# Optimization experiments

Hardware: AMD Instinct MI355X
Metric: run time of the kernel (lower is better)

Reference implementation:

```python
import jax, jax.numpy as jnp
import numpy as np

BLUR = 0.05
P = 2
EPS_FINAL = BLUR ** P          # geomloss: eps = blur**p = 0.0025
DIAMETER = 2.0                 # max cosine cost magnitude
SCALING = 0.5                  # geomloss default; eps decays by scaling**p per step
N_FINAL_ITERS = 4              # extra balancing iterations at the final eps


def eps_schedule():
    eps_list = []
    e = DIAMETER ** P
    while e > EPS_FINAL:
        eps_list.append(e)
        e = e * (SCALING ** P)
    eps_list.extend([EPS_FINAL] * N_FINAL_ITERS)
    return eps_list


def cosine_cost(a, b):
    # a: (N, D), b: (M, D) -> (N, M) cost = 1 - cos_sim
    an = a / (jnp.linalg.norm(a, axis=1, keepdims=True) + 1e-12)
    bn = b / (jnp.linalg.norm(b, axis=1, keepdims=True) + 1e-12)
    return 1.0 - an @ bn.T


def softmin(C, pot, log_w, eps):
    # -eps * LSE_j( log_w + (pot_j - C_ij)/eps ) ; C: (N, M), pot: (M,)
    return -eps * jax.nn.logsumexp(log_w + (pot[None, :] - C) / eps, axis=1)


def sinkhorn_divergence(Cxy, Cxx, Cyy):
    N, M = Cxy.shape
    log_a = -jnp.log(jnp.asarray(N, dtype=Cxy.dtype))  # uniform weights
    log_b = -jnp.log(jnp.asarray(M, dtype=Cxy.dtype))
    sg = jax.lax.stop_gradient
    # Sinkhorn iterations run on detached costs (geomloss envelope-theorem trick)
    Cxy_s, Cxx_s, Cyy_s = sg(Cxy), sg(Cxx), sg(Cyy)
    f = jnp.zeros((N,), Cxy.dtype)
    g = jnp.zeros((M,), Cxy.dtype)
    fxx = jnp.zeros((N,), Cxy.dtype)
    gyy = jnp.zeros((M,), Cxy.dtype)
    for eps in eps_schedule():
        # symmetric (debiasing) potentials: averaged fixed-point update
        fxx = 0.5 * (fxx + softmin(Cxx_s, fxx, log_a, eps))
        gyy = 0.5 * (gyy + softmin(Cyy_s, gyy, log_b, eps))
        # cross potentials: simultaneous (Jacobi) update
        f, g = softmin(Cxy_s, g, log_b, eps), softmin(Cxy_s.T, f, log_a, eps)
    # final extrapolation step with gradients flowing through the costs
    eps = EPS_FINAL
    f_fin = softmin(Cxy, sg(g), log_b, eps)
    g_fin = softmin(Cxy.T, sg(f), log_a, eps)
    fxx_fin = softmin(Cxx, sg(fxx), log_a, eps)
    gyy_fin = softmin(Cyy, sg(gyy), log_b, eps)
    return jnp.mean(f_fin - fxx_fin) + jnp.mean(g_fin - gyy_fin)


def setup_inputs() -> dict:
    key = jax.random.key(0)
    k1, k2, k3 = jax.random.split(key, 3)
    x1 = jax.random.normal(k1, (8192, 256), dtype=jnp.float32)
    x2 = jax.random.normal(k2, (8192, 256), dtype=jnp.float32)
    w = jax.random.uniform(k3, (256,), dtype=jnp.float32)
    return {"x1": x1, "x2": x2, "w": w}


def reference(x1, x2, w):
    # Dist_loss.forward: clamp+renormalize learned per-feature weights, scale x1
    w_c = jnp.clip(w, 0.0, 2.0)
    w_c = w_c / jnp.mean(w_c)
    a = w_c[None, :] * x1
    Cxy = cosine_cost(a, x2)
    Cxx = cosine_cost(a, a)
    Cyy = cosine_cost(x2, x2)
    return sinkhorn_divergence(Cxy, Cxx, Cyy)
```

## Files before the change

kernel.cpp:

```cpp
#include <hip/hip_runtime.h>
#include <math.h>

#define N 8192
#define D 256
#define LN2 0.6931471805599453f
#define LDSROW 280
#define TSLOTS 1152

typedef short short8 __attribute__((ext_vector_type(8)));
typedef float f32x16 __attribute__((ext_vector_type(16)));
typedef unsigned short ushort;

__device__ __forceinline__ float fexp2(float x) { return __builtin_amdgcn_exp2f(x); }
__device__ __forceinline__ float flog2(float x) { return __builtin_amdgcn_logf(x); }

__device__ __forceinline__ ushort bf16r(float x) {
    unsigned int u = __float_as_uint(x);
    return (ushort)((u + 0x7FFF + ((u >> 16) & 1)) >> 16);
}

__device__ __forceinline__ void gl_lds16(const ushort* g, ushort* l) {
    __builtin_amdgcn_global_load_lds(
        (const __attribute__((address_space(1))) unsigned int*)g,
        (__attribute__((address_space(3))) unsigned int*)l, 16, 0, 0);
}

__global__ void prep_wc(const float* __restrict__ w, float* __restrict__ wc) {
    int t = threadIdx.x;
    float v = fminf(fmaxf(w[t], 0.0f), 2.0f);
    float s = v;
#pragma unroll
    for (int m = 1; m < 64; m <<= 1) s += __shfl_xor(s, m);
    __shared__ float sm[4];
    if ((t & 63) == 0) sm[t >> 6] = s;
    __syncthreads();
    float mean = (sm[0] + sm[1] + sm[2] + sm[3]) * (1.0f / 256.0f);
    wc[t] = v / mean;
}

__global__ void prep_normalize(const float* __restrict__ x1, const float* __restrict__ x2,
                               const float* __restrict__ wc,
                               ushort* __restrict__ an_i, ushort* __restrict__ bn_i) {
    int row = blockIdx.x;
    int t = threadIdx.x;
    int r; float v; ushort* ip;
    if (row < N) { r = row;     v = x1[(size_t)r * D + t] * wc[t]; ip = an_i; }
    else         { r = row - N; v = x2[(size_t)r * D + t];         ip = bn_i; }
    float ss = v * v;
#pragma unroll
    for (int m = 1; m < 64; m <<= 1) ss += __shfl_xor(ss, m);
    __shared__ float sm[4];
    if ((t & 63) == 0) sm[t >> 6] = ss;
    __syncthreads();
    float denom = sqrtf(sm[0] + sm[1] + sm[2] + sm[3]) + 1e-12f;
    ip[(size_t)r * D + t] = bf16r(v / denom);
}

__global__ void init_pots(float* __restrict__ pots, float* __restrict__ potm1) {
    int id = blockIdx.x * 256 + threadIdx.x;
    pots[id] = 0.0f;
    potm1[id] = -1.0f;
}

__global__ __launch_bounds__(128, 2) void softmin_mfma(
    const ushort* __restrict__ an_i, const ushort* __restrict__ bn_i,
    const float* __restrict__ potm1,
    float2* __restrict__ parts, float k1) {
    int bx = blockIdx.x;
    int k = bx & 7;
    int q = bx >> 3;
    int task = k >> 1;
    int split = ((k & 1) << 1) | (q >> 6);
    int rb = q & 63;
    const ushort* jp = (task == 0 || task == 3) ? an_i : bn_i;
    const ushort* ip = (task == 0 || task == 2) ? an_i : bn_i;
    const float* pm1 = potm1 + (size_t)task * N;

    int t = threadIdx.x;
    int wave = t >> 6, lane = t & 63;
    int l31 = lane & 31, lh = lane >> 5;
    int i0 = rb * 128 + wave * 64;

    __shared__ ushort lbuf[2][TSLOTS * 8];

    short8 bi0[16], bi1[16];
    {
        const ushort* ib = ip + (size_t)(i0 + l31) * D + lh * 8;
#pragma unroll
        for (int c = 0; c < 16; ++c) {
            bi0[c] = *(const short8*)(ib + c * 16);
            bi1[c] = *(const short8*)(ib + (size_t)32 * D + c * 16);
        }
    }
#pragma unroll
    for (int c = 0; c < 16; ++c) {
        asm volatile("" : "+a"(bi0[c]), "+a"(bi1[c]));
    }

    const int jbase0 = split * 2048;

    int offA[9];
    int offP = 0;
    bool tail = false;
#pragma unroll
    for (int r = 0; r < 9; ++r) {
        int s = r * 128 + t;
        if (s >= 1120) {
            int u = s - 1120;
            offP = (u > 7 ? 7 : u) * 8;
            tail = true;
            offA[r] = 0;
        } else {
            int row = s / 35;
            int c = s - row * 35;
            c = c > 31 ? 31 : c;
            offA[r] = row * D + c * 8;
        }
    }

    auto stage = [&](int b, int js) {
        int j0 = jbase0 + js * 32;
        const ushort* gb = jp + (size_t)j0 * D;
        const ushort* gp = (const ushort*)(pm1 + j0);
        ushort* lb = &lbuf[b][0];
#pragma unroll
        for (int r = 0; r < 8; ++r)
            gl_lds16(gb + offA[r], lb + (r * 128 + t) * 8);
        gl_lds16(tail ? gp + offP : gb + offA[8], lb + (1024 + t) * 8);
    };

    auto tile = [&](const ushort* lb, f32x16& c0, f32x16& c1) {
        const float* pl = (const float*)(lb + 1120 * 8);
        float4 p0 = *(const float4*)&pl[4 * lh + 0];
        float4 p1 = *(const float4*)&pl[4 * lh + 8];
        float4 p2 = *(const float4*)&pl[4 * lh + 16];
        float4 p3 = *(const float4*)&pl[4 * lh + 24];
        c0[0] = p0.x; c0[1] = p0.y; c0[2]  = p0.z; c0[3]  = p0.w;
        c0[4] = p1.x; c0[5] = p1.y; c0[6]  = p1.z; c0[7]  = p1.w;
        c0[8] = p2.x; c0[9] = p2.y; c0[10] = p2.z; c0[11] = p2.w;
        c0[12] = p3.x; c0[13] = p3.y; c0[14] = p3.z; c0[15] = p3.w;
        c1 = c0;
        const ushort* lrow = lb + l31 * LDSROW + lh * 8;
        __builtin_amdgcn_s_setprio(1);
#pragma unroll
        for (int c = 0; c < 16; ++c) {
            short8 af = *(const short8*)(lrow + c * 16);
            c0 = __builtin_amdgcn_mfma_f32_32x32x16_bf16(af, bi0[c], c0, 0, 0, 0);
            c1 = __builtin_amdgcn_mfma_f32_32x32x16_bf16(af, bi1[c], c1, 0, 0, 0);
        }
        __builtin_amdgcn_s_setprio(0);
    };

    float m0 = -INFINITY, s0 = 0.0f, m1 = -INFINITY, s1 = 0.0f;

    auto lse = [&](const f32x16& c, float& m, float& s) {
        float a01 = fmaxf(c[0], c[1]),   a23 = fmaxf(c[2], c[3]);
        float a45 = fmaxf(c[4], c[5]),   a67 = fmaxf(c[6], c[7]);
        float a89 = fmaxf(c[8], c[9]),   aab = fmaxf(c[10], c[11]);
        float acd = fmaxf(c[12], c[13]), aef = fmaxf(c[14], c[15]);
        float q0 = fmaxf(a01, a23), q1 = fmaxf(a45, a67);
        float q2 = fmaxf(a89, aab), q3 = fmaxf(acd, aef);
        float mx = fmaxf(fmaxf(q0, q1), fmaxf(q2, q3));
        float mn = fmaxf(m, mx * k1);
        float nm = -mn;
        float t0 = fexp2(fmaf(c[0],  k1, nm)) + fexp2(fmaf(c[1],  k1, nm));
        float t1 = fexp2(fmaf(c[2],  k1, nm)) + fexp2(fmaf(c[3],  k1, nm));
        float t2 = fexp2(fmaf(c[4],  k1, nm)) + fexp2(fmaf(c[5],  k1, nm));
        float t3 = fexp2(fmaf(c[6],  k1, nm)) + fexp2(fmaf(c[7],  k1, nm));
        float t4 = fexp2(fmaf(c[8],  k1, nm)) + fexp2(fmaf(c[9],  k1, nm));
        float t5 = fexp2(fmaf(c[10], k1, nm)) + fexp2(fmaf(c[11], k1, nm));
        float t6 = fexp2(fmaf(c[12], k1, nm)) + fexp2(fmaf(c[13], k1, nm));
        float t7 = fexp2(fmaf(c[14], k1, nm)) + fexp2(fmaf(c[15], k1, nm));
        float ad = ((t0 + t1) + (t2 + t3)) + ((t4 + t5) + (t6 + t7));
        s = fmaf(s, fexp2(m - mn), ad);
        m = mn;
    };

    f32x16 a0, a1;

    stage(0, 0);
    for (int js = 0; js < 64; ++js) {
        int cur = js & 1;
        __syncthreads();
        if (js < 63) stage(cur ^ 1, js + 1);
        tile(&lbuf[cur][0], a0, a1);
        lse(a0, m0, s0);
        lse(a1, m1, s1);
    }

    float mo = __shfl_xor(m0, 32), so = __shfl_xor(s0, 32);
    float M0 = fmaxf(m0, mo);
    float S0 = s0 * fexp2(m0 - M0) + so * fexp2(mo - M0);
    mo = __shfl_xor(m1, 32); so = __shfl_xor(s1, 32);
    float M1 = fmaxf(m1, mo);
    float S1 = s1 * fexp2(m1 - M1) + so * fexp2(mo - M1);
    if (lane < 32) {
        size_t r0 = (size_t)task * N + (i0 + l31);
        size_t r1 = r0 + 32;
        parts[r0 * 4 + split] = make_float2(M0, S0);
        parts[r1 * 4 + split] = make_float2(M1, S1);
    }
}

__global__ void merge_pots(const float2* __restrict__ parts, float* __restrict__ pots,
                           float* __restrict__ potm1, float eps, float logw, int do_avg) {
    int id = blockIdx.x * 256 + threadIdx.x;
    int task = id >> 13;
    int row = id & (N - 1);
    const float2* p = parts + (size_t)id * 4;
    float2 a = p[0], b = p[1], c = p[2], d = p[3];
    float M = fmaxf(fmaxf(a.x, b.x), fmaxf(c.x, d.x));
    float S = a.y * fexp2(a.x - M) + b.y * fexp2(b.x - M) +
              c.y * fexp2(c.x - M) + d.y * fexp2(d.x - M);
    float lse = LN2 * (M + flog2(S));
    float v = -eps * (logw + lse);
    if (do_avg && task < 2) v = 0.5f * (pots[id] + v);
    pots[id] = v;
    int ct = (task < 2) ? task : (5 - task);
    potm1[(size_t)ct * N + row] = v - 1.0f;
}

__global__ void final_reduce(const float* __restrict__ pots, float* __restrict__ out) {
    int t = threadIdx.x;
    float s = 0.0f;
    for (int i = t; i < N; i += 256)
        s += (pots[2 * N + i] - pots[i]) + (pots[3 * N + i] - pots[N + i]);
#pragma unroll
    for (int m = 1; m < 64; m <<= 1) s += __shfl_xor(s, m);
    __shared__ float sm[4];
    if ((t & 63) == 0) sm[t >> 6] = s;
    __syncthreads();
    if (t == 0) out[0] = (sm[0] + sm[1] + sm[2] + sm[3]) * (1.0f / (float)N);
}

extern "C" void kernel_launch(void* const* d_in, const int* in_sizes, int n_in,
                              void* d_out, int out_size, void* d_ws, size_t ws_size,
                              hipStream_t stream) {
    const float* x1 = (const float*)d_in[0];
    const float* x2 = (const float*)d_in[1];
    const float* w  = (const float*)d_in[2];
    float* out = (float*)d_out;

    ushort* an_i = (ushort*)d_ws;
    ushort* bn_i = an_i + (size_t)N * D;
    float*  wc   = (float*)(bn_i + (size_t)N * D);
    float*  pots = wc + 256;
    float*  potm1 = pots + 4 * N;
    float2* parts = (float2*)(potm1 + 4 * N);

    prep_wc<<<1, 256, 0, stream>>>(w, wc);
    prep_normalize<<<2 * N, 256, 0, stream>>>(x1, x2, wc, an_i, bn_i);
    init_pots<<<4 * N / 256, 256, 0, stream>>>(pots, potm1);

    const float eps_list[10] = {4.0f, 1.0f, 0.25f, 0.0625f, 0.015625f,
                                0.00390625f, 0.0025f, 0.0025f, 0.0025f, 0.0025f};
    const float logw = -logf((float)N);
    const float LOG2E = 1.4426950408889634f;
    for (int it = 0; it < 10; ++it) {
        softmin_mfma<<<1024, 128, 0, stream>>>(an_i, bn_i, potm1, parts, LOG2E / eps_list[it]);
        merge_pots<<<4 * N / 256, 256, 0, stream>>>(parts, pots, potm1,
                                                    eps_list[it], logw, 1);
    }
    softmin_mfma<<<1024, 128, 0, stream>>>(an_i, bn_i, potm1, parts, LOG2E / 0.0025f);
    merge_pots<<<4 * N / 256, 256, 0, stream>>>(parts, pots, potm1, 0.0025f, logw, 0);
    final_reduce<<<1, 256, 0, stream>>>(pots, out);
}
```

Before: 1.683 ms.

## Warp-specialize softmin: MFMA waves write tiles to LDS, consumer waves do LSE

The block grows from 128 to 256 threads and the waves are split into two roles. Producer waves stage J tiles and run the MFMA matmul, then write the accumulator tiles into a double-buffered LDS region. Consumer waves read the previous tile from LDS and compute the streaming log-sum-exp. The goal is to overlap the exp-heavy LSE with matrix-core work across waves. The cost is extra LDS traffic, more shared memory per block and one extra pipeline step.

```diff
diff --git a/kernel.cpp b/kernel.cpp
--- a/kernel.cpp
+++ b/kernel.cpp
@@ -5,7 +5,7 @@
 #define D 256
 #define LN2 0.6931471805599453f
 #define LDSROW 280
-#define TSLOTS 1152
+#define JBUF_USH 9216
 
 typedef short short8 __attribute__((ext_vector_type(8)));
 typedef float f32x16 __attribute__((ext_vector_type(16)));
@@ -62,7 +62,7 @@
     potm1[id] = -1.0f;
 }
 
-__global__ __launch_bounds__(128, 2) void softmin_mfma(
+__global__ __launch_bounds__(256, 2) void softmin_mfma(
     const ushort* __restrict__ an_i, const ushort* __restrict__ bn_i,
     const float* __restrict__ potm1,
     float2* __restrict__ parts, float k1) {
@@ -79,54 +79,55 @@
     int t = threadIdx.x;
     int wave = t >> 6, lane = t & 63;
     int l31 = lane & 31, lh = lane >> 5;
-    int i0 = rb * 128 + wave * 64;
-
-    __shared__ ushort lbuf[2][TSLOTS * 8];
+    int pid = wave & 1;
+    int role = ((wave >> 1) ^ bx) & 1;
+    int i0 = rb * 128 + pid * 64;
+
+    __shared__ __attribute__((aligned(16))) ushort ldsA[38912];
+    float* accL = (float*)(ldsA + 2 * JBUF_USH);
+
+    const int jbase0 = split * 2048;
 
     short8 bi0[16], bi1[16];
-    {
+    int offA[9]; int offP = 0; bool tail = false;
+    int tp = pid * 64 + lane;
+
+    if (role == 0) {
         const ushort* ib = ip + (size_t)(i0 + l31) * D + lh * 8;
 #pragma unroll
         for (int c = 0; c < 16; ++c) {
             bi0[c] = *(const short8*)(ib + c * 16);
             bi1[c] = *(const short8*)(ib + (size_t)32 * D + c * 16);
         }
-    }
-#pragma unroll
-    for (int c = 0; c < 16; ++c) {
-        asm volatile("" : "+a"(bi0[c]), "+a"(bi1[c]));
-    }
-
-    const int jbase0 = split * 2048;
-
-    int offA[9];
-    int offP = 0;
-    bool tail = false;
-#pragma unroll
-    for (int r = 0; r < 9; ++r) {
-        int s = r * 128 + t;
-        if (s >= 1120) {
-            int u = s - 1120;
-            offP = (u > 7 ? 7 : u) * 8;
-            tail = true;
-            offA[r] = 0;
-        } else {
-            int row = s / 35;
-            int c = s - row * 35;
-            c = c > 31 ? 31 : c;
-            offA[r] = row * D + c * 8;
-        }
-    }
-
-    auto stage = [&](int b, int js) {
+#pragma unroll
+        for (int c = 0; c < 16; ++c) {
+            asm volatile("" : "+a"(bi0[c]), "+a"(bi1[c]));
+        }
+#pragma unroll
+        for (int r = 0; r < 9; ++r) {
+            int s = r * 128 + tp;
+            if (s >= 1120) {
+                int u = s - 1120;
+                offP = (u > 7 ? 7 : u) * 8;
+                tail = true;
+                offA[r] = 0;
+            } else {
+                int row = s / 35;
+                int c = s - row * 35;
+                c = c > 31 ? 31 : c;
+                offA[r] = row * D + c * 8;
+            }
+        }
+    }
+
+    auto stage = [&](ushort* lb, int js) {
         int j0 = jbase0 + js * 32;
         const ushort* gb = jp + (size_t)j0 * D;
         const ushort* gp = (const ushort*)(pm1 + j0);
-        ushort* lb = &lbuf[b][0];
 #pragma unroll
         for (int r = 0; r < 8; ++r)
-            gl_lds16(gb + offA[r], lb + (r * 128 + t) * 8);
-        gl_lds16(tail ? gp + offP : gb + offA[8], lb + (1024 + t) * 8);
+            gl_lds16(gb + offA[r], lb + (r * 128 + tp) * 8);
+        gl_lds16(tail ? gp + offP : gb + offA[8], lb + (1024 + tp) * 8);
     };
 
     auto tile = [&](const ushort* lb, f32x16& c0, f32x16& c1) {
@@ -151,54 +152,76 @@
         __builtin_amdgcn_s_setprio(0);
     };
 
-    float m0 = -INFINITY, s0 = 0.0f, m1 = -INFINITY, s1 = 0.0f;
-
-    auto lse = [&](const f32x16& c, float& m, float& s) {
-        float a01 = fmaxf(c[0], c[1]),   a23 = fmaxf(c[2], c[3]);
-        float a45 = fmaxf(c[4], c[5]),   a67 = fmaxf(c[6], c[7]);
-        float a89 = fmaxf(c[8], c[9]),   aab = fmaxf(c[10], c[11]);
-        float acd = fmaxf(c[12], c[13]), aef = fmaxf(c[14], c[15]);
-        float q0 = fmaxf(a01, a23), q1 = fmaxf(a45, a67);
-        float q2 = fmaxf(a89, aab), q3 = fmaxf(acd, aef);
-        float mx = fmaxf(fmaxf(q0, q1), fmaxf(q2, q3));
+    auto lse_l = [&](const float* lp, float& m, float& s) {
+        float4 v0 = *(const float4*)(lp + 0);
+        float4 v1 = *(const float4*)(lp + 4);
+        float4 v2 = *(const float4*)(lp + 8);
+        float4 v3 = *(const float4*)(lp + 12);
+        float g0 = fmaxf(fmaxf(v0.x, v0.y), v0.z);
+        float g1 = fmaxf(fmaxf(v0.w, v1.x), v1.y);
+        float g2 = fmaxf(fmaxf(v1.z, v1.w), v2.x);
+        float g3 = fmaxf(fmaxf(v2.y, v2.z), v2.w);
+        float g4 = fmaxf(fmaxf(v3.x, v3.y), v3.z);
+        float mx = fmaxf(fmaxf(fmaxf(g0, g1), g2), fmaxf(fmaxf(g3, g4), v3.w));
         float mn = fmaxf(m, mx * k1);
         float nm = -mn;
-        float t0 = fexp2(fmaf(c[0],  k1, nm)) + fexp2(fmaf(c[1],  k1, nm));
-        float t1 = fexp2(fmaf(c[2],  k1, nm)) + fexp2(fmaf(c[3],  k1, nm));
-        float t2 = fexp2(fmaf(c[4],  k1, nm)) + fexp2(fmaf(c[5],  k1, nm));
-        float t3 = fexp2(fmaf(c[6],  k1, nm)) + fexp2(fmaf(c[7],  k1, nm));
-        float t4 = fexp2(fmaf(c[8],  k1, nm)) + fexp2(fmaf(c[9],  k1, nm));
-        float t5 = fexp2(fmaf(c[10], k1, nm)) + fexp2(fmaf(c[11], k1, nm));
-        float t6 = fexp2(fmaf(c[12], k1, nm)) + fexp2(fmaf(c[13], k1, nm));
-        float t7 = fexp2(fmaf(c[14], k1, nm)) + fexp2(fmaf(c[15], k1, nm));
+        float t0 = fexp2(fmaf(v0.x, k1, nm)) + fexp2(fmaf(v0.y, k1, nm));
+        float t1 = fexp2(fmaf(v0.z, k1, nm)) + fexp2(fmaf(v0.w, k1, nm));
+        float t2 = fexp2(fmaf(v1.x, k1, nm)) + fexp2(fmaf(v1.y, k1, nm));
+        float t3 = fexp2(fmaf(v1.z, k1, nm)) + fexp2(fmaf(v1.w, k1, nm));
+        float t4 = fexp2(fmaf(v2.x, k1, nm)) + fexp2(fmaf(v2.y, k1, nm));
+        float t5 = fexp2(fmaf(v2.z, k1, nm)) + fexp2(fmaf(v2.w, k1, nm));
+        float t6 = fexp2(fmaf(v3.x, k1, nm)) + fexp2(fmaf(v3.y, k1, nm));
+        float t7 = fexp2(fmaf(v3.z, k1, nm)) + fexp2(fmaf(v3.w, k1, nm));
         float ad = ((t0 + t1) + (t2 + t3)) + ((t4 + t5) + (t6 + t7));
         s = fmaf(s, fexp2(m - mn), ad);
         m = mn;
     };
 
-    f32x16 a0, a1;
-
-    stage(0, 0);
-    for (int js = 0; js < 64; ++js) {
-        int cur = js & 1;
+    float* aw = accL + pid * 2560 + lane * 20;
+
+    float m0 = -INFINITY, s0 = 0.0f, m1 = -INFINITY, s1 = 0.0f;
+
+    if (role == 0) stage(ldsA, 0);
+    for (int s = 0; s <= 64; ++s) {
         __syncthreads();
-        if (js < 63) stage(cur ^ 1, js + 1);
-        tile(&lbuf[cur][0], a0, a1);
-        lse(a0, m0, s0);
-        lse(a1, m1, s1);
-    }
-
-    float mo = __shfl_xor(m0, 32), so = __shfl_xor(s0, 32);
-    float M0 = fmaxf(m0, mo);
-    float S0 = s0 * fexp2(m0 - M0) + so * fexp2(mo - M0);
-    mo = __shfl_xor(m1, 32); so = __shfl_xor(s1, 32);
-    float M1 = fmaxf(m1, mo);
-    float S1 = s1 * fexp2(m1 - M1) + so * fexp2(mo - M1);
-    if (lane < 32) {
-        size_t r0 = (size_t)task * N + (i0 + l31);
-        size_t r1 = r0 + 32;
-        parts[r0 * 4 + split] = make_float2(M0, S0);
-        parts[r1 * 4 + split] = make_float2(M1, S1);
+        if (role == 0) {
+            if (s < 64) {
+                ushort* lb = ldsA + (s & 1) * JBUF_USH;
+                if (s < 63) stage(ldsA + ((s + 1) & 1) * JBUF_USH, s + 1);
+                f32x16 c0, c1;
+                tile(lb, c0, c1);
+                float* w = aw + (s & 1) * 5120;
+                *(float4*)(w + 0)  = make_float4(c0[0],  c0[1],  c0[2],  c0[3]);
+                *(float4*)(w + 4)  = make_float4(c0[4],  c0[5],  c0[6],  c0[7]);
+                *(float4*)(w + 8)  = make_float4(c0[8],  c0[9],  c0[10], c0[11]);
+                *(float4*)(w + 12) = make_float4(c0[12], c0[13], c0[14], c0[15]);
+                float* w1 = w + 1280;
+                *(float4*)(w1 + 0)  = make_float4(c1[0],  c1[1],  c1[2],  c1[3]);
+                *(float4*)(w1 + 4)  = make_float4(c1[4],  c1[5],  c1[6],  c1[7]);
+                *(float4*)(w1 + 8)  = make_float4(c1[8],  c1[9],  c1[10], c1[11]);
+                *(float4*)(w1 + 12) = make_float4(c1[12], c1[13], c1[14], c1[15]);
+            }
+        } else if (s >= 1) {
+            const float* r = aw + ((s - 1) & 1) * 5120;
+            lse_l(r, m0, s0);
+            lse_l(r + 1280, m1, s1);
+        }
+    }
+
+    if (role == 1) {
+        float mo = __shfl_xor(m0, 32), so = __shfl_xor(s0, 32);
+        float M0 = fmaxf(m0, mo);
+        float S0 = s0 * fexp2(m0 - M0) + so * fexp2(mo - M0);
+        mo = __shfl_xor(m1, 32); so = __shfl_xor(s1, 32);
+        float M1 = fmaxf(m1, mo);
+        float S1 = s1 * fexp2(m1 - M1) + so * fexp2(mo - M1);
+        if (lane < 32) {
+            size_t r0 = (size_t)task * N + (i0 + l31);
+            size_t r1 = r0 + 32;
+            parts[r0 * 4 + split] = make_float2(M0, S0);
+            parts[r1 * 4 + split] = make_float2(M1, S1);
+        }
     }
 }
 
@@ -257,11 +280,11 @@
     const float logw = -logf((float)N);
     const float LOG2E = 1.4426950408889634f;
     for (int it = 0; it < 10; ++it) {
-        softmin_mfma<<<1024, 128, 0, stream>>>(an_i, bn_i, potm1, parts, LOG2E / eps_list[it]);
+        softmin_mfma<<<1024, 256, 0, stream>>>(an_i, bn_i, potm1, parts, LOG2E / eps_list[it]);
         merge_pots<<<4 * N / 256, 256, 0, stream>>>(parts, pots, potm1,
                                                     eps_list[it], logw, 1);
     }
-    softmin_mfma<<<1024, 128, 0, stream>>>(an_i, bn_i, potm1, parts, LOG2E / 0.0025f);
+    softmin_mfma<<<1024, 256, 0, stream>>>(an_i, bn_i, potm1, parts, LOG2E / 0.0025f);
     merge_pots<<<4 * N / 256, 256, 0, stream>>>(parts, pots, potm1, 0.0025f, logw, 0);
     final_reduce<<<1, 256, 0, stream>>>(pots, out);
 }
```

New measurement: 2.138 ms. +27.0%, slower.

## Pre-swizzle operands into MFMA fragment layout and load directly from global

Applied to the files above, without the earlier changes.

The normalize kernel now writes the bf16 matrices in a tiled layout that matches the MFMA operand fragments, so each lane can read its short8 fragments with coalesced global loads. The softmin kernel drops the LDS double-buffer, the global_load_lds staging and the per-tile barriers, and register-prefetches the next tile's A fragments and potentials while the current tile's LSE runs. Blocks grow to 256 threads covering 256 rows, so the grid halves. This removes LDS traffic and synchronisation, but each wave now fetches the shared j-tile separately through L1/L2, and the extra 16 prefetched fragment registers raise register pressure.

```diff
diff --git a/kernel.cpp b/kernel.cpp
--- a/kernel.cpp
+++ b/kernel.cpp
@@ -4,8 +4,6 @@
 #define N 8192
 #define D 256
 #define LN2 0.6931471805599453f
-#define LDSROW 280
-#define TSLOTS 1152
 
 typedef short short8 __attribute__((ext_vector_type(8)));
 typedef float f32x16 __attribute__((ext_vector_type(16)));
@@ -19,12 +17,6 @@
     return (ushort)((u + 0x7FFF + ((u >> 16) & 1)) >> 16);
 }
 
-__device__ __forceinline__ void gl_lds16(const ushort* g, ushort* l) {
-    __builtin_amdgcn_global_load_lds(
-        (const __attribute__((address_space(1))) unsigned int*)g,
-        (__attribute__((address_space(3))) unsigned int*)l, 16, 0, 0);
-}
-
 __global__ void prep_wc(const float* __restrict__ w, float* __restrict__ wc) {
     int t = threadIdx.x;
     float v = fminf(fmaxf(w[t], 0.0f), 2.0f);
@@ -40,12 +32,12 @@
 
 __global__ void prep_normalize(const float* __restrict__ x1, const float* __restrict__ x2,
                                const float* __restrict__ wc,
-                               ushort* __restrict__ an_i, ushort* __restrict__ bn_i) {
+                               ushort* __restrict__ an_t, ushort* __restrict__ bn_t) {
     int row = blockIdx.x;
     int t = threadIdx.x;
     int r; float v; ushort* ip;
-    if (row < N) { r = row;     v = x1[(size_t)r * D + t] * wc[t]; ip = an_i; }
-    else         { r = row - N; v = x2[(size_t)r * D + t];         ip = bn_i; }
+    if (row < N) { r = row;     v = x1[(size_t)r * D + t] * wc[t]; ip = an_t; }
+    else         { r = row - N; v = x2[(size_t)r * D + t];         ip = bn_t; }
     float ss = v * v;
 #pragma unroll
     for (int m = 1; m < 64; m <<= 1) ss += __shfl_xor(ss, m);
@@ -53,7 +45,15 @@
     if ((t & 63) == 0) sm[t >> 6] = ss;
     __syncthreads();
     float denom = sqrtf(sm[0] + sm[1] + sm[2] + sm[3]) + 1e-12f;
-    ip[(size_t)r * D + t] = bf16r(v / denom);
+    __shared__ __attribute__((aligned(16))) ushort ls[256];
+    ls[t] = bf16r(v / denom);
+    __syncthreads();
+    if (t < 32) {
+        int c = t >> 1, lh = t & 1;
+        short8 vv = *(const short8*)&ls[c * 16 + lh * 8];
+        size_t base = (size_t)(r >> 5) * 8192 + (size_t)c * 512 + lh * 256 + (r & 31) * 8;
+        *(short8*)(ip + base) = vv;
+    }
 }
 
 __global__ void init_pots(float* __restrict__ pots, float* __restrict__ potm1) {
@@ -62,34 +62,32 @@
     potm1[id] = -1.0f;
 }
 
-__global__ __launch_bounds__(128, 2) void softmin_mfma(
-    const ushort* __restrict__ an_i, const ushort* __restrict__ bn_i,
+__global__ __launch_bounds__(256, 2) void softmin_mfma(
+    const ushort* __restrict__ an_t, const ushort* __restrict__ bn_t,
     const float* __restrict__ potm1,
     float2* __restrict__ parts, float k1) {
     int bx = blockIdx.x;
     int k = bx & 7;
     int q = bx >> 3;
     int task = k >> 1;
-    int split = ((k & 1) << 1) | (q >> 6);
-    int rb = q & 63;
-    const ushort* jp = (task == 0 || task == 3) ? an_i : bn_i;
-    const ushort* ip = (task == 0 || task == 2) ? an_i : bn_i;
+    int split = ((k & 1) << 1) | (q & 1);
+    int rb = q >> 1;
+    const ushort* jp = (task == 0 || task == 3) ? an_t : bn_t;
+    const ushort* ip = (task == 0 || task == 2) ? an_t : bn_t;
     const float* pm1 = potm1 + (size_t)task * N;
 
     int t = threadIdx.x;
     int wave = t >> 6, lane = t & 63;
     int l31 = lane & 31, lh = lane >> 5;
-    int i0 = rb * 128 + wave * 64;
-
-    __shared__ ushort lbuf[2][TSLOTS * 8];
+    int i0 = rb * 256 + wave * 64;
 
     short8 bi0[16], bi1[16];
     {
-        const ushort* ib = ip + (size_t)(i0 + l31) * D + lh * 8;
+        const ushort* ib = ip + (size_t)(i0 >> 5) * 8192 + lane * 8;
 #pragma unroll
         for (int c = 0; c < 16; ++c) {
-            bi0[c] = *(const short8*)(ib + c * 16);
-            bi1[c] = *(const short8*)(ib + (size_t)32 * D + c * 16);
+            bi0[c] = *(const short8*)(ib + c * 512);
+            bi1[c] = *(const short8*)(ib + 8192 + c * 512);
         }
     }
 #pragma unroll
@@ -98,69 +96,39 @@
     }
 
     const int jbase0 = split * 2048;
-
-    int offA[9];
-    int offP = 0;
-    bool tail = false;
-#pragma unroll
-    for (int r = 0; r < 9; ++r) {
-        int s = r * 128 + t;
-        if (s >= 1120) {
-            int u = s - 1120;
-            offP = (u > 7 ? 7 : u) * 8;
-            tail = true;
-            offA[r] = 0;
-        } else {
-            int row = s / 35;
-            int c = s - row * 35;
-            c = c > 31 ? 31 : c;
-            offA[r] = row * D + c * 8;
-        }
-    }
-
-    auto stage = [&](int b, int js) {
-        int j0 = jbase0 + js * 32;
-        const ushort* gb = jp + (size_t)j0 * D;
-        const ushort* gp = (const ushort*)(pm1 + j0);
-        ushort* lb = &lbuf[b][0];
-#pragma unroll
-        for (int r = 0; r < 8; ++r)
-            gl_lds16(gb + offA[r], lb + (r * 128 + t) * 8);
-        gl_lds16(tail ? gp + offP : gb + offA[8], lb + (1024 + t) * 8);
+    const ushort* ab = jp + (size_t)(jbase0 >> 5) * 8192 + lane * 8;
+    const float*  pb = pm1 + jbase0 + 4 * lh;
+
+    f32x16 c0, c1;
+    short8 af[16];
+
+    auto ldaf = [&]() {
+#pragma unroll
+        for (int c = 0; c < 16; ++c)
+            af[c] = *(const short8*)(ab + c * 512);
     };
-
-    auto tile = [&](const ushort* lb, f32x16& c0, f32x16& c1) {
-        const float* pl = (const float*)(lb + 1120 * 8);
-        float4 p0 = *(const float4*)&pl[4 * lh + 0];
-        float4 p1 = *(const float4*)&pl[4 * lh + 8];
-        float4 p2 = *(const float4*)&pl[4 * lh + 16];
-        float4 p3 = *(const float4*)&pl[4 * lh + 24];
+    auto ldpot = [&]() {
+        float4 p0 = *(const float4*)(pb + 0);
+        float4 p1 = *(const float4*)(pb + 8);
+        float4 p2 = *(const float4*)(pb + 16);
+        float4 p3 = *(const float4*)(pb + 24);
         c0[0] = p0.x; c0[1] = p0.y; c0[2]  = p0.z; c0[3]  = p0.w;
         c0[4] = p1.x; c0[5] = p1.y; c0[6]  = p1.z; c0[7]  = p1.w;
         c0[8] = p2.x; c0[9] = p2.y; c0[10] = p2.z; c0[11] = p2.w;
         c0[12] = p3.x; c0[13] = p3.y; c0[14] = p3.z; c0[15] = p3.w;
         c1 = c0;
-        const ushort* lrow = lb + l31 * LDSROW + lh * 8;
-        __builtin_amdgcn_s_setprio(1);
-#pragma unroll
-        for (int c = 0; c < 16; ++c) {
-            short8 af = *(const short8*)(lrow + c * 16);
-            c0 = __builtin_amdgcn_mfma_f32_32x32x16_bf16(af, bi0[c], c0, 0, 0, 0);
-            c1 = __builtin_amdgcn_mfma_f32_32x32x16_bf16(af, bi1[c], c1, 0, 0, 0);
-        }
-        __builtin_amdgcn_s_setprio(0);
     };
 
     float m0 = -INFINITY, s0 = 0.0f, m1 = -INFINITY, s1 = 0.0f;
 
     auto lse = [&](const f32x16& c, float& m, float& s) {
-        float a01 = fmaxf(c[0], c[1]),   a23 = fmaxf(c[2], c[3]);
-        float a45 = fmaxf(c[4], c[5]),   a67 = fmaxf(c[6], c[7]);
-        float a89 = fmaxf(c[8], c[9]),   aab = fmaxf(c[10], c[11]);
-        float acd = fmaxf(c[12], c[13]), aef = fmaxf(c[14], c[15]);
-        float q0 = fmaxf(a01, a23), q1 = fmaxf(a45, a67);
-        float q2 = fmaxf(a89, aab), q3 = fmaxf(acd, aef);
-        float mx = fmaxf(fmaxf(q0, q1), fmaxf(q2, q3));
+        float g0 = fmaxf(fmaxf(c[0],  c[1]),  c[2]);
+        float g1 = fmaxf(fmaxf(c[3],  c[4]),  c[5]);
+        float g2 = fmaxf(fmaxf(c[6],  c[7]),  c[8]);
+        float g3 = fmaxf(fmaxf(c[9],  c[10]), c[11]);
+        float g4 = fmaxf(fmaxf(c[12], c[13]), c[14]);
+        float h  = fmaxf(fmaxf(g0, g1), g2);
+        float mx = fmaxf(fmaxf(h, g3), fmaxf(g4, c[15]));
         float mn = fmaxf(m, mx * k1);
         float nm = -mn;
         float t0 = fexp2(fmaf(c[0],  k1, nm)) + fexp2(fmaf(c[1],  k1, nm));
@@ -176,16 +144,23 @@
         m = mn;
     };
 
-    f32x16 a0, a1;
-
-    stage(0, 0);
+    ldpot();
+    ldaf();
     for (int js = 0; js < 64; ++js) {
-        int cur = js & 1;
-        __syncthreads();
-        if (js < 63) stage(cur ^ 1, js + 1);
-        tile(&lbuf[cur][0], a0, a1);
-        lse(a0, m0, s0);
-        lse(a1, m1, s1);
+        __builtin_amdgcn_s_setprio(1);
+#pragma unroll
+        for (int c = 0; c < 16; ++c) {
+            short8 a = af[c];
+            c0 = __builtin_amdgcn_mfma_f32_32x32x16_bf16(a, bi0[c], c0, 0, 0, 0);
+            c1 = __builtin_amdgcn_mfma_f32_32x32x16_bf16(a, bi1[c], c1, 0, 0, 0);
+        }
+        __builtin_amdgcn_s_setprio(0);
+        ab += 8192;
+        if (js < 63) ldaf();
+        lse(c0, m0, s0);
+        lse(c1, m1, s1);
+        pb += 32;
+        if (js < 63) ldpot();
     }
 
     float mo = __shfl_xor(m0, 32), so = __shfl_xor(s0, 32);
@@ -241,15 +216,15 @@
     const float* w  = (const float*)d_in[2];
     float* out = (float*)d_out;
 
-    ushort* an_i = (ushort*)d_ws;
-    ushort* bn_i = an_i + (size_t)N * D;
-    float*  wc   = (float*)(bn_i + (size_t)N * D);
+    ushort* an_t = (ushort*)d_ws;
+    ushort* bn_t = an_t + (size_t)N * D;
+    float*  wc   = (float*)(bn_t + (size_t)N * D);
     float*  pots = wc + 256;
     float*  potm1 = pots + 4 * N;
     float2* parts = (float2*)(potm1 + 4 * N);
 
     prep_wc<<<1, 256, 0, stream>>>(w, wc);
-    prep_normalize<<<2 * N, 256, 0, stream>>>(x1, x2, wc, an_i, bn_i);
+    prep_normalize<<<2 * N, 256, 0, stream>>>(x1, x2, wc, an_t, bn_t);
     init_pots<<<4 * N / 256, 256, 0, stream>>>(pots, potm1);
 
     const float eps_list[10] = {4.0f, 1.0f, 0.25f, 0.0625f, 0.015625f,
@@ -257,11 +232,11 @@
     const float logw = -logf((float)N);
     const float LOG2E = 1.4426950408889634f;
     for (int it = 0; it < 10; ++it) {
-        softmin_mfma<<<1024, 128, 0, stream>>>(an_i, bn_i, potm1, parts, LOG2E / eps_list[it]);
+        softmin_mfma<<<512, 256, 0, stream>>>(an_t, bn_t, potm1, parts, LOG2E / eps_list[it]);
         merge_pots<<<4 * N / 256, 256, 0, stream>>>(parts, pots, potm1,
                                                     eps_list[it], logw, 1);
     }
-    softmin_mfma<<<1024, 128, 0, stream>>>(an_i, bn_i, potm1, parts, LOG2E / 0.0025f);
+    softmin_mfma<<<512, 256, 0, stream>>>(an_t, bn_t, potm1, parts, LOG2E / 0.0025f);
     merge_pots<<<4 * N / 256, 256, 0, stream>>>(parts, pots, potm1, 0.0025f, logw, 0);
     final_reduce<<<1, 256, 0, stream>>>(pots, out);
 }
```

New measurement: 1.793 ms. 6.6% more time.

## Enlarge softmin blocks to 8 waves, split MFMA chains, stagger LSE across wave groups

Applied to the files above, without the earlier changes.

Blocks grow from 128 to 512 threads (8 waves, 512 i-rows each), so each LDS-staged j tile is shared by four times as many waves and the grid shrinks to 256 blocks. The 16-step MFMA accumulation is split into two independent chains that are summed at the end, which shortens the dependency latency. Half the waves run their exp/LSE for the previous tile before issuing the next MFMAs, so matrix and vector work from different waves can interleave. The cost is more registers and fewer blocks in flight, and with only 256 blocks some CUs may sit idle.

```diff
diff --git a/kernel.cpp b/kernel.cpp
--- a/kernel.cpp
+++ b/kernel.cpp
@@ -62,7 +62,7 @@
     potm1[id] = -1.0f;
 }
 
-__global__ __launch_bounds__(128, 2) void softmin_mfma(
+__global__ __launch_bounds__(512, 2) void softmin_mfma(
     const ushort* __restrict__ an_i, const ushort* __restrict__ bn_i,
     const float* __restrict__ potm1,
     float2* __restrict__ parts, float k1) {
@@ -70,8 +70,8 @@
     int k = bx & 7;
     int q = bx >> 3;
     int task = k >> 1;
-    int split = ((k & 1) << 1) | (q >> 6);
-    int rb = q & 63;
+    int split = ((k & 1) << 1) | (q >> 4);
+    int rb = q & 15;
     const ushort* jp = (task == 0 || task == 3) ? an_i : bn_i;
     const ushort* ip = (task == 0 || task == 2) ? an_i : bn_i;
     const float* pm1 = potm1 + (size_t)task * N;
@@ -79,7 +79,8 @@
     int t = threadIdx.x;
     int wave = t >> 6, lane = t & 63;
     int l31 = lane & 31, lh = lane >> 5;
-    int i0 = rb * 128 + wave * 64;
+    int ga = (wave >> 2) == 0;
+    int i0 = rb * 512 + wave * 64;
 
     __shared__ ushort lbuf[2][TSLOTS * 8];
 
@@ -99,12 +100,12 @@
 
     const int jbase0 = split * 2048;
 
-    int offA[9];
+    int offA[3];
     int offP = 0;
     bool tail = false;
 #pragma unroll
-    for (int r = 0; r < 9; ++r) {
-        int s = r * 128 + t;
+    for (int r = 0; r < 3; ++r) {
+        int s = (r < 2) ? (r * 512 + t) : (1024 + (t & 127));
         if (s >= 1120) {
             int u = s - 1120;
             offP = (u > 7 ? 7 : u) * 8;
@@ -123,32 +124,48 @@
         const ushort* gb = jp + (size_t)j0 * D;
         const ushort* gp = (const ushort*)(pm1 + j0);
         ushort* lb = &lbuf[b][0];
-#pragma unroll
-        for (int r = 0; r < 8; ++r)
-            gl_lds16(gb + offA[r], lb + (r * 128 + t) * 8);
-        gl_lds16(tail ? gp + offP : gb + offA[8], lb + (1024 + t) * 8);
+        gl_lds16(gb + offA[0], lb + t * 8);
+        gl_lds16(gb + offA[1], lb + (512 + t) * 8);
+        gl_lds16(tail ? gp + offP : gb + offA[2], lb + (1024 + (t & 127)) * 8);
     };
 
-    auto tile = [&](const ushort* lb, f32x16& c0, f32x16& c1) {
+    f32x16 zz = {};
+    asm volatile("" : "+v"(zz));
+
+    auto chainsum = [&](const ushort* lb, f32x16& p0, f32x16& p1) {
         const float* pl = (const float*)(lb + 1120 * 8);
-        float4 p0 = *(const float4*)&pl[4 * lh + 0];
-        float4 p1 = *(const float4*)&pl[4 * lh + 8];
-        float4 p2 = *(const float4*)&pl[4 * lh + 16];
-        float4 p3 = *(const float4*)&pl[4 * lh + 24];
-        c0[0] = p0.x; c0[1] = p0.y; c0[2]  = p0.z; c0[3]  = p0.w;
-        c0[4] = p1.x; c0[5] = p1.y; c0[6]  = p1.z; c0[7]  = p1.w;
-        c0[8] = p2.x; c0[9] = p2.y; c0[10] = p2.z; c0[11] = p2.w;
-        c0[12] = p3.x; c0[13] = p3.y; c0[14] = p3.z; c0[15] = p3.w;
-        c1 = c0;
+        f32x16 pt;
+        float4 q0 = *(const float4*)&pl[4 * lh + 0];
+        float4 q1 = *(const float4*)&pl[4 * lh + 8];
+        float4 q2 = *(const float4*)&pl[4 * lh + 16];
+        float4 q3 = *(const float4*)&pl[4 * lh + 24];
+        pt[0] = q0.x; pt[1] = q0.y; pt[2]  = q0.z; pt[3]  = q0.w;
+        pt[4] = q1.x; pt[5] = q1.y; pt[6]  = q1.z; pt[7]  = q1.w;
+        pt[8] = q2.x; pt[9] = q2.y; pt[10] = q2.z; pt[11] = q2.w;
+        pt[12] = q3.x; pt[13] = q3.y; pt[14] = q3.z; pt[15] = q3.w;
         const ushort* lrow = lb + l31 * LDSROW + lh * 8;
+        f32x16 c0a, c0b, c1a, c1b;
         __builtin_amdgcn_s_setprio(1);
-#pragma unroll
-        for (int c = 0; c < 16; ++c) {
-            short8 af = *(const short8*)(lrow + c * 16);
-            c0 = __builtin_amdgcn_mfma_f32_32x32x16_bf16(af, bi0[c], c0, 0, 0, 0);
-            c1 = __builtin_amdgcn_mfma_f32_32x32x16_bf16(af, bi1[c], c1, 0, 0, 0);
+        {
+            short8 alo = *(const short8*)(lrow + 0);
+            short8 ahi = *(const short8*)(lrow + 8 * 16);
+            c0a = __builtin_amdgcn_mfma_f32_32x32x16_bf16(alo, bi0[0], pt, 0, 0, 0);
+            c1a = __builtin_amdgcn_mfma_f32_32x32x16_bf16(alo, bi1[0], pt, 0, 0, 0);
+            c0b = __builtin_amdgcn_mfma_f32_32x32x16_bf16(ahi, bi0[8], zz, 0, 0, 0);
+            c1b = __builtin_amdgcn_mfma_f32_32x32x16_bf16(ahi, bi1[8], zz, 0, 0, 0);
+        }
+#pragma unroll
+        for (int c = 1; c < 8; ++c) {
+            short8 alo = *(const short8*)(lrow + c * 16);
+            short8 ahi = *(const short8*)(lrow + (c + 8) * 16);
+            c0a = __builtin_amdgcn_mfma_f32_32x32x16_bf16(alo, bi0[c], c0a, 0, 0, 0);
+            c1a = __builtin_amdgcn_mfma_f32_32x32x16_bf16(alo, bi1[c], c1a, 0, 0, 0);
+            c0b = __builtin_amdgcn_mfma_f32_32x32x16_bf16(ahi, bi0[c + 8], c0b, 0, 0, 0);
+            c1b = __builtin_amdgcn_mfma_f32_32x32x16_bf16(ahi, bi1[c + 8], c1b, 0, 0, 0);
         }
         __builtin_amdgcn_s_setprio(0);
+        p0 = c0a + c0b;
+        p1 = c1a + c1b;
     };
 
     float m0 = -INFINITY, s0 = 0.0f, m1 = -INFINITY, s1 = 0.0f;
@@ -176,16 +193,28 @@
         m = mn;
     };
 
-    f32x16 a0, a1;
+    f32x16 p0, p1;
 
     stage(0, 0);
     for (int js = 0; js < 64; ++js) {
         int cur = js & 1;
         __syncthreads();
         if (js < 63) stage(cur ^ 1, js + 1);
-        tile(&lbuf[cur][0], a0, a1);
-        lse(a0, m0, s0);
-        lse(a1, m1, s1);
+        if (ga) {
+            chainsum(&lbuf[cur][0], p0, p1);
+            lse(p0, m0, s0);
+            lse(p1, m1, s1);
+        } else {
+            if (js) {
+                lse(p0, m0, s0);
+                lse(p1, m1, s1);
+            }
+            chainsum(&lbuf[cur][0], p0, p1);
+        }
+    }
+    if (!ga) {
+        lse(p0, m0, s0);
+        lse(p1, m1, s1);
     }
 
     float mo = __shfl_xor(m0, 32), so = __shfl_xor(s0, 32);
@@ -257,11 +286,11 @@
     const float logw = -logf((float)N);
     const float LOG2E = 1.4426950408889634f;
     for (int it = 0; it < 10; ++it) {
-        softmin_mfma<<<1024, 128, 0, stream>>>(an_i, bn_i, potm1, parts, LOG2E / eps_list[it]);
+        softmin_mfma<<<256, 512, 0, stream>>>(an_i, bn_i, potm1, parts, LOG2E / eps_list[it]);
         merge_pots<<<4 * N / 256, 256, 0, stream>>>(parts, pots, potm1,
                                                     eps_list[it], logw, 1);
     }
-    softmin_mfma<<<1024, 128, 0, stream>>>(an_i, bn_i, potm1, parts, LOG2E / 0.0025f);
+    softmin_mfma<<<256, 512, 0, stream>>>(an_i, bn_i, potm1, parts, LOG2E / 0.0025f);
     merge_pots<<<4 * N / 256, 256, 0, stream>>>(parts, pots, potm1, 0.0025f, logw, 0);
     final_reduce<<<1, 256, 0, stream>>>(pots, out);
 }
```

Result: slower. 3.085 ms (+83.3%).
